# Kernel tuning notes

Measured on AMD Instinct MI355X. Metric: run time of the kernel, lower is better.

The kernel has to match this reference:

```python
import jax, jax.numpy as jnp
import numpy as np

N_HOST, N_FLOW, E = 20000, 200000, 600000
D_IN, D_H, D_OUT = 64, 128, 32
NEG_SLOPE = 0.01  # F.leaky_relu default


def setup_inputs() -> dict:
    key = jax.random.key(0)
    ks = jax.random.split(key, 20)

    def w(k, shape):
        # kaiming-uniform-ish init scale (matches Linear fan-in scaling)
        lim = 1.0 / np.sqrt(shape[0])
        return jax.random.uniform(k, shape, jnp.float32, -lim, lim)

    return {
        "x_host": jax.random.normal(ks[0], (N_HOST, D_IN), jnp.float32),
        "x_flow": jax.random.normal(ks[1], (N_FLOW, D_IN), jnp.float32),
        "src_hf": jax.random.randint(ks[2], (E,), 0, N_HOST, dtype=jnp.int32),
        "dst_hf": jax.random.randint(ks[3], (E,), 0, N_FLOW, dtype=jnp.int32),
        "src_fh": jax.random.randint(ks[4], (E,), 0, N_FLOW, dtype=jnp.int32),
        "dst_fh": jax.random.randint(ks[5], (E,), 0, N_HOST, dtype=jnp.int32),
        "W0_hf_l": w(ks[6], (D_IN, D_H)), "W0_hf_r": w(ks[7], (D_IN, D_H)),
        "b0_hf": jnp.zeros((D_H,), jnp.float32),
        "W0_fh_l": w(ks[8], (D_IN, D_H)), "W0_fh_r": w(ks[9], (D_IN, D_H)),
        "b0_fh": jnp.zeros((D_H,), jnp.float32),
        "W1_hf_l": w(ks[10], (D_H, D_H)), "W1_hf_r": w(ks[11], (D_H, D_H)),
        "b1_hf": jnp.zeros((D_H,), jnp.float32),
        "W1_fh_l": w(ks[12], (D_H, D_H)), "W1_fh_r": w(ks[13], (D_H, D_H)),
        "b1_fh": jnp.zeros((D_H,), jnp.float32),
        "W_out": w(ks[14], (D_H, D_OUT)),
        "b_out": jnp.zeros((D_OUT,), jnp.float32),
    }


def _seg_mean(x, src, dst, n_dst):
    """Mean-aggregate src-node features over edges into n_dst segments."""
    s = jax.ops.segment_sum(x[src], dst, num_segments=n_dst)      # [n_dst, d]
    cnt = jax.ops.segment_sum(jnp.ones(src.shape, x.dtype), dst, num_segments=n_dst)
    return s / jnp.clip(cnt, 1.0)[:, None]


def _sage(x_src, x_dst, src, dst, Wl, Wr, b, n_dst):
    # SAGEConv: lin_l(mean_agg) + bias + lin_r(x_dst)
    agg = _seg_mean(x_src, src, dst, n_dst)
    return agg @ Wl + b + x_dst @ Wr


def reference(x_host, x_flow, src_hf, dst_hf, src_fh, dst_fh,
              W0_hf_l, W0_hf_r, b0_hf, W0_fh_l, W0_fh_r, b0_fh,
              W1_hf_l, W1_hf_r, b1_hf, W1_fh_l, W1_fh_r, b1_fh,
              W_out, b_out):
    lrelu = lambda v: jnp.where(v > 0, v, NEG_SLOPE * v)

    # layer 0
    h_flow = lrelu(_sage(x_host, x_flow, src_hf, dst_hf, W0_hf_l, W0_hf_r, b0_hf, N_FLOW))
    h_host = lrelu(_sage(x_flow, x_host, src_fh, dst_fh, W0_fh_l, W0_fh_r, b0_fh, N_HOST))

    # layer 1
    g_flow = lrelu(_sage(h_host, h_flow, src_hf, dst_hf, W1_hf_l, W1_hf_r, b1_hf, N_FLOW))
    g_host = lrelu(_sage(h_flow, h_host, src_fh, dst_fh, W1_fh_l, W1_fh_r, b1_fh, N_HOST))
    del g_host  # computed (matches module) but only 'flow' feeds the head

    return g_flow @ W_out + b_out  # [N_FLOW, D_OUT]
```

## Files before the change

### kernel.cpp

```cpp
#include <hip/hip_runtime.h>


#define N_HOST 20000
#define N_FLOW 200000
#define NEDGE  600000
#define D_IN   64
#define D_H    128
#define D_OUT  32
#define NSEG   (N_FLOW + N_HOST)
#define NBKT_F 196
#define NBKT_H 79
#define NBKT   (NBKT_F + NBKT_H)
#define NEB    586

typedef unsigned short u16;
typedef unsigned int   u32;
typedef short bf16x8 __attribute__((ext_vector_type(8)));
typedef float f32x4  __attribute__((ext_vector_type(4)));

__device__ __forceinline__ float bfh(u16 h) { return __uint_as_float(((u32)h) << 16); }
__device__ __forceinline__ u16 fbh(float f) {
    u32 u = __float_as_uint(f);
    return (u16)((u + 0x7fffu + ((u >> 16) & 1u)) >> 16);
}
__device__ __forceinline__ u32 packbf(float x, float y) {
    return (u32)fbh(x) | ((u32)fbh(y) << 16);
}
__device__ __forceinline__ void acc8(float* a, uint4 u) {
    a[0] += __uint_as_float(u.x << 16);
    a[1] += __uint_as_float(u.x & 0xffff0000u);
    a[2] += __uint_as_float(u.y << 16);
    a[3] += __uint_as_float(u.y & 0xffff0000u);
    a[4] += __uint_as_float(u.z << 16);
    a[5] += __uint_as_float(u.z & 0xffff0000u);
    a[6] += __uint_as_float(u.w << 16);
    a[7] += __uint_as_float(u.w & 0xffff0000u);
}

__device__ __forceinline__ uint4 gmean(const u16* __restrict__ pool, int rs, int coff,
                                       const int* __restrict__ gcsr,
                                       const int* __restrict__ lcsr, int st0, bool fit,
                                       int st, int en) {
    float a[8] = {0.f, 0.f, 0.f, 0.f, 0.f, 0.f, 0.f, 0.f};
    for (int e = st; e < en; e += 4) {
        int n[4];
#pragma unroll
        for (int j = 0; j < 4; j++)
            n[j] = (e + j < en) ? (fit ? lcsr[e + j - st0] : gcsr[e + j]) : -1;
        uint4 u[4];
#pragma unroll
        for (int j = 0; j < 4; j++)
            u[j] = (n[j] >= 0) ? *(const uint4*)(pool + n[j] * rs + coff)
                               : make_uint4(0u, 0u, 0u, 0u);
#pragma unroll
        for (int j = 0; j < 4; j++) acc8(a, u[j]);
    }
    float inv = (en > st) ? 1.f / (float)(en - st) : 0.f;
    uint4 o;
    o.x = packbf(a[0] * inv, a[1] * inv);
    o.y = packbf(a[2] * inv, a[3] * inv);
    o.z = packbf(a[4] * inv, a[5] * inv);
    o.w = packbf(a[6] * inv, a[7] * inv);
    return o;
}

__global__ void k_pre(const float* __restrict__ W0_hf_l, const float* __restrict__ W0_hf_r,
                      const float* __restrict__ W0_fh_l, const float* __restrict__ W0_fh_r,
                      const float* __restrict__ W1_l, const float* __restrict__ W1_r,
                      const float* __restrict__ Wout,
                      u16* __restrict__ WT0_hf, u16* __restrict__ WT0_fh,
                      u16* __restrict__ WT1_l, u16* __restrict__ WT1_r,
                      u16* __restrict__ WTo,
                      const float* __restrict__ xf, const float* __restrict__ xh,
                      u16* __restrict__ xfb, u16* __restrict__ xhb,
                      const int* __restrict__ dst_hf, const int* __restrict__ dst_fh,
                      int* __restrict__ bcnt) {
    int b = blockIdx.x, t = threadIdx.x;
    if (b < 34) {
        u16 tmp[8];
        if (b < 32) {
            int e = (b & 7) * 2048 + t * 8;
            int n = e >> 7, k0 = e & 127;
            if (b < 8) {
#pragma unroll
                for (int j = 0; j < 8; j++) {
                    int k = k0 + j;
                    tmp[j] = fbh(k < 64 ? W0_hf_l[k * D_H + n] : W0_hf_r[(k - 64) * D_H + n]);
                }
                *(uint4*)(WT0_hf + n * 128 + k0) = *(uint4*)tmp;
            } else if (b < 16) {
#pragma unroll
                for (int j = 0; j < 8; j++) {
                    int k = k0 + j;
                    tmp[j] = fbh(k < 64 ? W0_fh_l[k * D_H + n] : W0_fh_r[(k - 64) * D_H + n]);
                }
                *(uint4*)(WT0_fh + n * 128 + k0) = *(uint4*)tmp;
            } else if (b < 24) {
#pragma unroll
                for (int j = 0; j < 8; j++) tmp[j] = fbh(W1_l[(k0 + j) * D_H + n]);
                *(uint4*)(WT1_l + n * 128 + k0) = *(uint4*)tmp;
            } else {
#pragma unroll
                for (int j = 0; j < 8; j++) tmp[j] = fbh(W1_r[(k0 + j) * D_H + n]);
                *(uint4*)(WT1_r + n * 128 + k0) = *(uint4*)tmp;
            }
        } else {
            int e = (b - 32) * 2048 + t * 8;
            int n = e >> 7, k0 = e & 127;
#pragma unroll
            for (int j = 0; j < 8; j++) tmp[j] = fbh(Wout[(k0 + j) * D_OUT + n]);
            *(uint4*)(WTo + n * 128 + k0) = *(uint4*)tmp;
        }
    } else if (b < 34 + 6875) {
        int q = (b - 34) * 256 + t;
        const int TF = (N_FLOW * D_IN) / 8;
        const int TT = TF + (N_HOST * D_IN) / 8;
        if (q >= TT) return;
        const float* src; u16* dst; int base;
        if (q < TF) { src = xf; dst = xfb; base = q * 8; }
        else        { src = xh; dst = xhb; base = (q - TF) * 8; }
        float4 f0 = *(const float4*)(src + base);
        float4 f1 = *(const float4*)(src + base + 4);
        uint4 o;
        o.x = packbf(f0.x, f0.y); o.y = packbf(f0.z, f0.w);
        o.z = packbf(f1.x, f1.y); o.w = packbf(f1.z, f1.w);
        *(uint4*)(dst + base) = o;
    } else {
        __shared__ int h[NBKT];
        for (int j = t; j < NBKT; j += 256) h[j] = 0;
        __syncthreads();
        int base = (b - 34 - 6875) * 2048;
#pragma unroll
        for (int i = 0; i < 8; i++) {
            int e = base + t + i * 256;
            if (e < 2 * NEDGE) {
                int bkt = (e < NEDGE) ? (dst_hf[e] >> 10)
                                      : (NBKT_F + (dst_fh[e - NEDGE] >> 8));
                atomicAdd(&h[bkt], 1);
            }
        }
        __syncthreads();
        for (int j = t; j < NBKT; j += 256)
            if (h[j]) atomicAdd(&bcnt[j], h[j]);
    }
}

__global__ void kb2(const int* __restrict__ src_hf, const int* __restrict__ dst_hf,
                    const int* __restrict__ src_fh, const int* __restrict__ dst_fh,
                    const int* __restrict__ bcnt, int* __restrict__ bcur,
                    int2* __restrict__ binE) {
    __shared__ int sp[512];
    __shared__ int lh[NBKT];
    __shared__ int lb[NBKT];
    int t = threadIdx.x;
    int o1 = (t < NBKT) ? bcnt[t] : 0;
    int o2 = (t + 256 < NBKT) ? bcnt[t + 256] : 0;
    sp[t] = o1; sp[t + 256] = o2;
    for (int j = t; j < NBKT; j += 256) lh[j] = 0;
    __syncthreads();
    for (int d = 1; d < 512; d <<= 1) {
        int a0 = (t >= d) ? sp[t - d] : 0;
        int a1 = sp[t + 256 - d];
        __syncthreads();
        sp[t] += a0; sp[t + 256] += a1;
        __syncthreads();
    }
    sp[t] -= o1; sp[t + 256] -= o2;
    __syncthreads();
    int base = blockIdx.x * 2048;
    int mybkt[8], myrank[8], mysrc[8], mydst[8];
#pragma unroll
    for (int i = 0; i < 8; i++) {
        int e = base + t + i * 256;
        mybkt[i] = -1;
        if (e < 2 * NEDGE) {
            int s, d;
            if (e < NEDGE) { s = src_hf[e]; d = dst_hf[e]; }
            else           { s = src_fh[e - NEDGE]; d = dst_fh[e - NEDGE] + N_FLOW; }
            int bkt = (d < N_FLOW) ? (d >> 10) : (NBKT_F + ((d - N_FLOW) >> 8));
            mybkt[i] = bkt; mysrc[i] = s; mydst[i] = d;
            myrank[i] = atomicAdd(&lh[bkt], 1);
        }
    }
    __syncthreads();
    for (int j = t; j < NBKT; j += 256)
        lb[j] = lh[j] ? atomicAdd(&bcur[j], lh[j]) : 0;
    __syncthreads();
#pragma unroll
    for (int i = 0; i < 8; i++) {
        if (mybkt[i] >= 0) {
            int pos = sp[mybkt[i]] + lb[mybkt[i]] + myrank[i];
            binE[pos] = make_int2(mysrc[i], mydst[i]);
        }
    }
}

__global__ __launch_bounds__(256) void kb3(const int2* __restrict__ binE,
                                           const int* __restrict__ bcnt,
                                           int* __restrict__ off, int* __restrict__ csr) {
    __shared__ int sp[512];
    __shared__ int deg[1024];
    __shared__ int ts[256];
    int b = blockIdx.x, t = threadIdx.x;
    sp[t] = (t < NBKT) ? bcnt[t] : 0;
    sp[t + 256] = (t + 256 < NBKT) ? bcnt[t + 256] : 0;
    __syncthreads();
    for (int d = 1; d < 512; d <<= 1) {
        int a0 = (t >= d) ? sp[t - d] : 0;
        int a1 = sp[t + 256 - d];
        __syncthreads();
        sp[t] += a0; sp[t + 256] += a1;
        __syncthreads();
    }
    int e0 = (b == 0) ? 0 : sp[b - 1];
    int e1 = sp[b];
    int nbase, ncnt;
    if (b < NBKT_F) { nbase = b << 10; ncnt = min(1024, N_FLOW - nbase); }
    else { nbase = N_FLOW + ((b - NBKT_F) << 8); ncnt = min(256, NSEG - nbase); }
    for (int i = t; i < 1024; i += 256) deg[i] = 0;
    __syncthreads();
    for (int e = e0 + t; e < e1; e += 256) {
        int2 p = binE[e];
        atomicAdd(&deg[p.y - nbase], 1);
    }
    __syncthreads();
    int loc[4]; int s = 0;
#pragma unroll
    for (int j = 0; j < 4; j++) { loc[j] = s; s += deg[t * 4 + j]; }
    ts[t] = s;
    __syncthreads();
    for (int d = 1; d < 256; d <<= 1) {
        int x = (t >= d) ? ts[t - d] : 0;
        __syncthreads();
        ts[t] += x;
        __syncthreads();
    }
    int base2 = e0 + ts[t] - s;
    int dsave[4];
#pragma unroll
    for (int j = 0; j < 4; j++) dsave[j] = deg[t * 4 + j];
    __syncthreads();
#pragma unroll
    for (int j = 0; j < 4; j++) {
        int idx = t * 4 + j;
        int st = base2 + loc[j];
        deg[idx] = st;
        if (idx < ncnt) off[nbase + idx] = st + dsave[j];
    }
    __syncthreads();
    for (int e = e0 + t; e < e1; e += 256) {
        int2 p = binE[e];
        int r = atomicAdd(&deg[p.y - nbase], 1);
        csr[r] = p.x;
    }
}

__global__ __launch_bounds__(256) void k_host(
    const u16* __restrict__ xfb, const u16* __restrict__ xhb,
    const int* __restrict__ off, const int* __restrict__ csr,
    const u16* __restrict__ WT0, const float* __restrict__ b0,
    const u16* __restrict__ WT1l, u16* __restrict__ hT, int M) {
    __shared__ __align__(16) u16 sA[64 * 136];
    __shared__ int sOff[72];
    __shared__ int sCsr[2560];
    const int t = threadIdx.x;
    const int m0 = blockIdx.x * 64;
    if (t < 65) {
        int idx = N_FLOW + m0 - 1 + t;
        sOff[t] = off[min(idx, NSEG - 1)];
    }
#pragma unroll
    for (int i = 0; i < 2; i++) {
        int q = t + i * 256;
        int r = q >> 3, c = q & 7;
        int row = m0 + r;
        uint4 v = make_uint4(0u, 0u, 0u, 0u);
        if (row < M) v = *(const uint4*)(xhb + row * 64 + c * 8);
        *(uint4*)(&sA[r * 136 + 64 + c * 8]) = v;
    }
    __syncthreads();
    int st0 = sOff[0];
    int win = sOff[64] - st0;
    bool fit = (win <= 2560);
    if (fit) for (int e = t; e < win; e += 256) sCsr[e] = csr[st0 + e];
    __syncthreads();
#pragma unroll
    for (int i = 0; i < 2; i++) {
        int q = t + i * 256;
        int r = q >> 3, c = q & 7;
        int row = m0 + r;
        uint4 o = make_uint4(0u, 0u, 0u, 0u);
        if (row < M) o = gmean(xfb, 64, c * 8, csr, sCsr, st0, fit, sOff[r], sOff[r + 1]);
        *(uint4*)(&sA[r * 136 + c * 8]) = o;
    }
    __syncthreads();
    const int w = t >> 6, ln = t & 63, l15 = ln & 15, quad = ln >> 4;
    const u16* pA = sA + (w * 16 + l15) * 136 + quad * 8;
    const u16* pB0 = WT0 + l15 * 128 + quad * 8;
    f32x4 acc[8];
#pragma unroll
    for (int tt = 0; tt < 8; tt++) acc[tt] = (f32x4){0.f, 0.f, 0.f, 0.f};
#pragma unroll
    for (int s = 0; s < 4; s++) {
        bf16x8 a = *(const bf16x8*)(pA + s * 32);
#pragma unroll
        for (int tt = 0; tt < 8; tt++) {
            bf16x8 b = *(const bf16x8*)(pB0 + tt * 2048 + s * 32);
            acc[tt] = __builtin_amdgcn_mfma_f32_16x16x32_bf16(a, b, acc[tt], 0, 0, 0);
        }
    }
#pragma unroll
    for (int tt = 0; tt < 8; tt++) {
        int col = tt * 16 + l15;
        float bv = b0[col];
#pragma unroll
        for (int i = 0; i < 4; i++) {
            int rl = w * 16 + quad * 4 + i;
            float v = acc[tt][i] + bv;
            v = v > 0.f ? v : 0.01f * v;
            sA[rl * 136 + col] = fbh(v);
        }
    }
    const u16* pB1 = WT1l + l15 * 128 + quad * 8;
    f32x4 accB[8];
#pragma unroll
    for (int tt = 0; tt < 8; tt++) accB[tt] = (f32x4){0.f, 0.f, 0.f, 0.f};
#pragma unroll
    for (int s = 0; s < 4; s++) {
        bf16x8 a = *(const bf16x8*)(pA + s * 32);
#pragma unroll
        for (int tt = 0; tt < 8; tt++) {
            bf16x8 b = *(const bf16x8*)(pB1 + tt * 2048 + s * 32);
            accB[tt] = __builtin_amdgcn_mfma_f32_16x16x32_bf16(a, b, accB[tt], 0, 0, 0);
        }
    }
#pragma unroll
    for (int tt = 0; tt < 8; tt++) {
        int col = tt * 16 + l15;
#pragma unroll
        for (int i = 0; i < 4; i++) {
            int row = m0 + w * 16 + quad * 4 + i;
            if (row < M) hT[row * D_H + col] = fbh(accB[tt][i]);
        }
    }
}

__global__ __launch_bounds__(256) void k_mega(
    const u16* __restrict__ xfb, const u16* __restrict__ xhb,
    const int* __restrict__ off, const int* __restrict__ csr,
    const u16* __restrict__ hT,
    const u16* __restrict__ WT0, const float* __restrict__ b0,
    const u16* __restrict__ WT1r, const float* __restrict__ b1,
    const u16* __restrict__ WTo, const float* __restrict__ bout,
    float* __restrict__ OUT) {
    __shared__ __align__(16) u16 sA[64 * 136];
    __shared__ __align__(16) u16 sAg[64 * 136];
    __shared__ int sOff[72];
    __shared__ int sCsr[1024];
    const int t = threadIdx.x;
    const int m0 = blockIdx.x * 64;
    if (t < 65) {
        int idx = m0 - 1 + t;
        sOff[t] = (idx < 0) ? 0 : off[idx];
    }
#pragma unroll
    for (int i = 0; i < 2; i++) {
        int q = t + i * 256;
        int r = q >> 3, c = q & 7;
        int row = m0 + r;
        uint4 v = *(const uint4*)(xfb + row * 64 + c * 8);
        *(uint4*)(&sA[r * 136 + 64 + c * 8]) = v;
    }
    __syncthreads();
    int st0 = sOff[0];
    int win = sOff[64] - st0;
    bool fit = (win <= 1024);
    if (fit) for (int e = t; e < win; e += 256) sCsr[e] = csr[st0 + e];
    __syncthreads();
#pragma unroll
    for (int i = 0; i < 2; i++) {
        int q = t + i * 256;
        int r = q >> 3, c = q & 7;
        uint4 o = gmean(xhb, 64, c * 8, csr, sCsr, st0, fit, sOff[r], sOff[r + 1]);
        *(uint4*)(&sA[r * 136 + c * 8]) = o;
    }
#pragma unroll
    for (int i = 0; i < 4; i++) {
        int q = t + i * 256;
        int r = q >> 4, c = q & 15;
        uint4 o = gmean(hT, 128, c * 8, csr, sCsr, st0, fit, sOff[r], sOff[r + 1]);
        *(uint4*)(&sAg[r * 136 + c * 8]) = o;
    }
    __syncthreads();
    const int w = t >> 6, ln = t & 63, l15 = ln & 15, quad = ln >> 4;
    const u16* pA = sA + (w * 16 + l15) * 136 + quad * 8;
    const u16* pB0 = WT0 + l15 * 128 + quad * 8;
    f32x4 acc[8];
#pragma unroll
    for (int tt = 0; tt < 8; tt++) acc[tt] = (f32x4){0.f, 0.f, 0.f, 0.f};
#pragma unroll
    for (int s = 0; s < 4; s++) {
        bf16x8 a = *(const bf16x8*)(pA + s * 32);
#pragma unroll
        for (int tt = 0; tt < 8; tt++) {
            bf16x8 b = *(const bf16x8*)(pB0 + tt * 2048 + s * 32);
            acc[tt] = __builtin_amdgcn_mfma_f32_16x16x32_bf16(a, b, acc[tt], 0, 0, 0);
        }
    }
#pragma unroll
    for (int tt = 0; tt < 8; tt++) {
        int col = tt * 16 + l15;
        float bv = b0[col];
#pragma unroll
        for (int i = 0; i < 4; i++) {
            int rl = w * 16 + quad * 4 + i;
            float v = acc[tt][i] + bv;
            v = v > 0.f ? v : 0.01f * v;
            sA[rl * 136 + col] = fbh(v);
        }
    }
    const u16* pB1 = WT1r + l15 * 128 + quad * 8;
    f32x4 accB[8];
#pragma unroll
    for (int tt = 0; tt < 8; tt++) accB[tt] = (f32x4){0.f, 0.f, 0.f, 0.f};
#pragma unroll
    for (int s = 0; s < 4; s++) {
        bf16x8 a = *(const bf16x8*)(pA + s * 32);
#pragma unroll
        for (int tt = 0; tt < 8; tt++) {
            bf16x8 b = *(const bf16x8*)(pB1 + tt * 2048 + s * 32);
            accB[tt] = __builtin_amdgcn_mfma_f32_16x16x32_bf16(a, b, accB[tt], 0, 0, 0);
        }
    }
#pragma unroll
    for (int tt = 0; tt < 8; tt++) {
        int col = tt * 16 + l15;
        float bv = b1[col];
#pragma unroll
        for (int i = 0; i < 4; i++) {
            int rl = w * 16 + quad * 4 + i;
            float v = accB[tt][i] + bfh(sAg[rl * 136 + col]) + bv;
            v = v > 0.f ? v : 0.01f * v;
            sA[rl * 136 + col] = fbh(v);
        }
    }
    const u16* pBo = WTo + l15 * 128 + quad * 8;
    f32x4 acc2[2];
    acc2[0] = (f32x4){0.f, 0.f, 0.f, 0.f};
    acc2[1] = (f32x4){0.f, 0.f, 0.f, 0.f};
#pragma unroll
    for (int s = 0; s < 4; s++) {
        bf16x8 g = *(const bf16x8*)(pA + s * 32);
        acc2[0] = __builtin_amdgcn_mfma_f32_16x16x32_bf16(g, *(const bf16x8*)(pBo + s * 32), acc2[0], 0, 0, 0);
        acc2[1] = __builtin_amdgcn_mfma_f32_16x16x32_bf16(g, *(const bf16x8*)(pBo + 2048 + s * 32), acc2[1], 0, 0, 0);
    }
#pragma unroll
    for (int tt = 0; tt < 2; tt++) {
        int col = tt * 16 + l15;
        float bv = bout[col];
#pragma unroll
        for (int i = 0; i < 4; i++) {
            int row = m0 + w * 16 + quad * 4 + i;
            OUT[row * D_OUT + col] = acc2[tt][i] + bv;
        }
    }
}

extern "C" void kernel_launch(void* const* d_in, const int* in_sizes, int n_in,
                              void* d_out, int out_size, void* d_ws, size_t ws_size,
                              hipStream_t stream) {
    const float* x_host  = (const float*)d_in[0];
    const float* x_flow  = (const float*)d_in[1];
    const int* src_hf  = (const int*)d_in[2];
    const int* dst_hf  = (const int*)d_in[3];
    const int* src_fh  = (const int*)d_in[4];
    const int* dst_fh  = (const int*)d_in[5];
    const float* W0_hf_l = (const float*)d_in[6];
    const float* W0_hf_r = (const float*)d_in[7];
    const float* b0_hf   = (const float*)d_in[8];
    const float* W0_fh_l = (const float*)d_in[9];
    const float* W0_fh_r = (const float*)d_in[10];
    const float* b0_fh   = (const float*)d_in[11];
    const float* W1_hf_l = (const float*)d_in[12];
    const float* W1_hf_r = (const float*)d_in[13];
    const float* b1_hf   = (const float*)d_in[14];
    const float* W_out   = (const float*)d_in[18];
    const float* b_out   = (const float*)d_in[19];
    float* out = (float*)d_out;

    char* ws = (char*)d_ws;
    int*  off    = (int*)(ws + 0);
    int*  csr    = (int*)(ws + 880000);
    u16*  hT     = (u16*)(ws + 5680000);
    u16*  xfb    = (u16*)(ws + 10800000);
    u16*  xhb    = (u16*)(ws + 36400000);
    int2* binE   = (int2*)(ws + 38960000);
    int*  bcnt   = (int*)(ws + 48560000);
    int*  bcur   = (int*)(ws + 48561280);
    u16*  WT0_hf = (u16*)(ws + 48562560);
    u16*  WT0_fh = (u16*)(ws + 48595328);
    u16*  WT1_l  = (u16*)(ws + 48628096);
    u16*  WT1_r  = (u16*)(ws + 48660864);
    u16*  WTo    = (u16*)(ws + 48693632);

    hipMemsetAsync(bcnt, 0, 2560, stream);
    k_pre<<<34 + 6875 + NEB, 256, 0, stream>>>(
        W0_hf_l, W0_hf_r, W0_fh_l, W0_fh_r, W1_hf_l, W1_hf_r, W_out,
        WT0_hf, WT0_fh, WT1_l, WT1_r, WTo,
        x_flow, x_host, xfb, xhb, dst_hf, dst_fh, bcnt);
    kb2<<<NEB, 256, 0, stream>>>(src_hf, dst_hf, src_fh, dst_fh, bcnt, bcur, binE);
    kb3<<<NBKT, 256, 0, stream>>>(binE, bcnt, off, csr);
    k_host<<<313, 256, 0, stream>>>(xfb, xhb, off, csr, WT0_fh, b0_fh, WT1_l, hT, N_HOST);
    k_mega<<<3125, 256, 0, stream>>>(xfb, xhb, off, csr, hT, WT0_hf, b0_hf,
                                     WT1_r, b1_hf, WTo, b_out, out);
}
```

Before: 355.7 us.

## Double threads per block in host and flow kernels, split GEMM columns across warps

Both fused kernels move from 256 to 512 threads per 64-row tile. Each thread now gathers one 8-column chunk instead of looping over two, and the 8 waves are laid out as 4 row groups by 2 column halves for the MFMA stages. The goal is more memory-level parallelism in the irregular gather phase and more resident waves to hide latency. The cost is extra __syncthreads between stages, because column-split waves now write shared rows that other waves read. The host kernel's gather unroll is also raised to 8.

```diff
diff --git a/kernel.cpp b/kernel.cpp
--- a/kernel.cpp
+++ b/kernel.cpp
@@ -37,23 +37,24 @@
     a[7] += __uint_as_float(u.w & 0xffff0000u);
 }
 
+template <int U>
 __device__ __forceinline__ uint4 gmean(const u16* __restrict__ pool, int rs, int coff,
                                        const int* __restrict__ gcsr,
                                        const int* __restrict__ lcsr, int st0, bool fit,
                                        int st, int en) {
     float a[8] = {0.f, 0.f, 0.f, 0.f, 0.f, 0.f, 0.f, 0.f};
-    for (int e = st; e < en; e += 4) {
-        int n[4];
-#pragma unroll
-        for (int j = 0; j < 4; j++)
+    for (int e = st; e < en; e += U) {
+        int n[U];
+#pragma unroll
+        for (int j = 0; j < U; j++)
             n[j] = (e + j < en) ? (fit ? lcsr[e + j - st0] : gcsr[e + j]) : -1;
-        uint4 u[4];
-#pragma unroll
-        for (int j = 0; j < 4; j++)
+        uint4 u[U];
+#pragma unroll
+        for (int j = 0; j < U; j++)
             u[j] = (n[j] >= 0) ? *(const uint4*)(pool + n[j] * rs + coff)
                                : make_uint4(0u, 0u, 0u, 0u);
 #pragma unroll
-        for (int j = 0; j < 4; j++) acc8(a, u[j]);
+        for (int j = 0; j < U; j++) acc8(a, u[j]);
     }
     float inv = (en > st) ? 1.f / (float)(en - st) : 0.f;
     uint4 o;
@@ -255,7 +256,7 @@
     }
 }
 
-__global__ __launch_bounds__(256) void k_host(
+__global__ __launch_bounds__(512, 4) void k_host(
     const u16* __restrict__ xfb, const u16* __restrict__ xhb,
     const int* __restrict__ off, const int* __restrict__ csr,
     const u16* __restrict__ WT0, const float* __restrict__ b0,
@@ -269,10 +270,8 @@
         int idx = N_FLOW + m0 - 1 + t;
         sOff[t] = off[min(idx, NSEG - 1)];
     }
-#pragma unroll
-    for (int i = 0; i < 2; i++) {
-        int q = t + i * 256;
-        int r = q >> 3, c = q & 7;
+    {
+        int r = t >> 3, c = t & 7;
         int row = m0 + r;
         uint4 v = make_uint4(0u, 0u, 0u, 0u);
         if (row < M) v = *(const uint4*)(xhb + row * 64 + c * 8);
@@ -282,70 +281,71 @@
     int st0 = sOff[0];
     int win = sOff[64] - st0;
     bool fit = (win <= 2560);
-    if (fit) for (int e = t; e < win; e += 256) sCsr[e] = csr[st0 + e];
-    __syncthreads();
-#pragma unroll
-    for (int i = 0; i < 2; i++) {
-        int q = t + i * 256;
-        int r = q >> 3, c = q & 7;
+    if (fit) for (int e = t; e < win; e += 512) sCsr[e] = csr[st0 + e];
+    __syncthreads();
+    {
+        int r = t >> 3, c = t & 7;
         int row = m0 + r;
         uint4 o = make_uint4(0u, 0u, 0u, 0u);
-        if (row < M) o = gmean(xfb, 64, c * 8, csr, sCsr, st0, fit, sOff[r], sOff[r + 1]);
+        if (row < M) o = gmean<8>(xfb, 64, c * 8, csr, sCsr, st0, fit, sOff[r], sOff[r + 1]);
         *(uint4*)(&sA[r * 136 + c * 8]) = o;
     }
     __syncthreads();
-    const int w = t >> 6, ln = t & 63, l15 = ln & 15, quad = ln >> 4;
-    const u16* pA = sA + (w * 16 + l15) * 136 + quad * 8;
-    const u16* pB0 = WT0 + l15 * 128 + quad * 8;
-    f32x4 acc[8];
-#pragma unroll
-    for (int tt = 0; tt < 8; tt++) acc[tt] = (f32x4){0.f, 0.f, 0.f, 0.f};
+    const int w = t >> 6, wr = w >> 1, wc = w & 1;
+    const int ln = t & 63, l15 = ln & 15, quad = ln >> 4;
+    const u16* pA = sA + (wr * 16 + l15) * 136 + quad * 8;
+    const u16* pB0 = WT0 + wc * 8192 + l15 * 128 + quad * 8;
+    f32x4 acc[4];
+#pragma unroll
+    for (int tt = 0; tt < 4; tt++) acc[tt] = (f32x4){0.f, 0.f, 0.f, 0.f};
 #pragma unroll
     for (int s = 0; s < 4; s++) {
         bf16x8 a = *(const bf16x8*)(pA + s * 32);
 #pragma unroll
-        for (int tt = 0; tt < 8; tt++) {
+        for (int tt = 0; tt < 4; tt++) {
             bf16x8 b = *(const bf16x8*)(pB0 + tt * 2048 + s * 32);
             acc[tt] = __builtin_amdgcn_mfma_f32_16x16x32_bf16(a, b, acc[tt], 0, 0, 0);
         }
     }
-#pragma unroll
-    for (int tt = 0; tt < 8; tt++) {
-        int col = tt * 16 + l15;
+    __syncthreads();
+#pragma unroll
+    for (int tt = 0; tt < 4; tt++) {
+        int col = wc * 64 + tt * 16 + l15;
         float bv = b0[col];
 #pragma unroll
         for (int i = 0; i < 4; i++) {
-            int rl = w * 16 + quad * 4 + i;
+            int rl = wr * 16 + quad * 4 + i;
             float v = acc[tt][i] + bv;
             v = v > 0.f ? v : 0.01f * v;
             sA[rl * 136 + col] = fbh(v);
         }
     }
-    const u16* pB1 = WT1l + l15 * 128 + quad * 8;
-    f32x4 accB[8];
-#pragma unroll
-    for (int tt = 0; tt < 8; tt++) accB[tt] = (f32x4){0.f, 0.f, 0.f, 0.f};
+    __syncthreads();
+    const u16* pB1 = WT1l + wc * 8192 + l15 * 128 + quad * 8;
+    f32x4 accB[4];
+#pragma unroll
+    for (int tt = 0; tt < 4; tt++) accB[tt] = (f32x4){0.f, 0.f, 0.f, 0.f};
 #pragma unroll
     for (int s = 0; s < 4; s++) {
         bf16x8 a = *(const bf16x8*)(pA + s * 32);
 #pragma unroll
-        for (int tt = 0; tt < 8; tt++) {
+        for (int tt = 0; tt < 4; tt++) {
             bf16x8 b = *(const bf16x8*)(pB1 + tt * 2048 + s * 32);
             accB[tt] = __builtin_amdgcn_mfma_f32_16x16x32_bf16(a, b, accB[tt], 0, 0, 0);
         }
     }
 #pragma unroll
-    for (int tt = 0; tt < 8; tt++) {
-        int col = tt * 16 + l15;
+    for (int tt = 0; tt < 4; tt++) {
+        int col = wc * 64 + tt * 16 + l15;
 #pragma unroll
         for (int i = 0; i < 4; i++) {
-            int row = m0 + w * 16 + quad * 4 + i;
+            int row = m0 + wr * 16 + quad * 4 + i;
             if (row < M) hT[row * D_H + col] = fbh(accB[tt][i]);
         }
     }
 }
 
-__global__ __launch_bounds__(256) void k_mega(
+__global__ __launch_bounds__(512, 8) void k_mega(
     const u16* __restrict__ xfb, const u16* __restrict__ xhb,
     const int* __restrict__ off, const int* __restrict__ csr,
     const u16* __restrict__ hT,
@@ -363,105 +363,102 @@
         int idx = m0 - 1 + t;
         sOff[t] = (idx < 0) ? 0 : off[idx];
     }
-#pragma unroll
-    for (int i = 0; i < 2; i++) {
-        int q = t + i * 256;
-        int r = q >> 3, c = q & 7;
-        int row = m0 + r;
-        uint4 v = *(const uint4*)(xfb + row * 64 + c * 8);
+    {
+        int r = t >> 3, c = t & 7;
+        uint4 v = *(const uint4*)(xfb + (m0 + r) * 64 + c * 8);
         *(uint4*)(&sA[r * 136 + 64 + c * 8]) = v;
     }
     __syncthreads();
     int st0 = sOff[0];
     int win = sOff[64] - st0;
     bool fit = (win <= 1024);
-    if (fit) for (int e = t; e < win; e += 256) sCsr[e] = csr[st0 + e];
-    __syncthreads();
+    if (fit) for (int e = t; e < win; e += 512) sCsr[e] = csr[st0 + e];
+    __syncthreads();
+    {
+        int r = t >> 3, c = t & 7;
+        uint4 o = gmean<4>(xhb, 64, c * 8, csr, sCsr, st0, fit, sOff[r], sOff[r + 1]);
+        *(uint4*)(&sA[r * 136 + c * 8]) = o;
+    }
 #pragma unroll
     for (int i = 0; i < 2; i++) {
-        int q = t + i * 256;
-        int r = q >> 3, c = q & 7;
-        uint4 o = gmean(xhb, 64, c * 8, csr, sCsr, st0, fit, sOff[r], sOff[r + 1]);
-        *(uint4*)(&sA[r * 136 + c * 8]) = o;
-    }
-#pragma unroll
-    for (int i = 0; i < 4; i++) {
-        int q = t + i * 256;
+        int q = t + i * 512;
         int r = q >> 4, c = q & 15;
-        uint4 o = gmean(hT, 128, c * 8, csr, sCsr, st0, fit, sOff[r], sOff[r + 1]);
+        uint4 o = gmean<4>(hT, 128, c * 8, csr, sCsr, st0, fit, sOff[r], sOff[r + 1]);
         *(uint4*)(&sAg[r * 136 + c * 8]) = o;
     }
     __syncthreads();
-    const int w = t >> 6, ln = t & 63, l15 = ln & 15, quad = ln >> 4;
-    const u16* pA = sA + (w * 16 + l15) * 136 + quad * 8;
-    const u16* pB0 = WT0 + l15 * 128 + quad * 8;
-    f32x4 acc[8];
-#pragma unroll
-    for (int tt = 0; tt < 8; tt++) acc[tt] = (f32x4){0.f, 0.f, 0.f, 0.f};
+    const int w = t >> 6, wr = w >> 1, wc = w & 1;
+    const int ln = t & 63, l15 = ln & 15, quad = ln >> 4;
+    const u16* pA = sA + (wr * 16 + l15) * 136 + quad * 8;
+    const u16* pB0 = WT0 + wc * 8192 + l15 * 128 + quad * 8;
+    f32x4 acc[4];
+#pragma unroll
+    for (int tt = 0; tt < 4; tt++) acc[tt] = (f32x4){0.f, 0.f, 0.f, 0.f};
 #pragma unroll
     for (int s = 0; s < 4; s++) {
         bf16x8 a = *(const bf16x8*)(pA + s * 32);
 #pragma unroll
-        for (int tt = 0; tt < 8; tt++) {
+        for (int tt = 0; tt < 4; tt++) {
             bf16x8 b = *(const bf16x8*)(pB0 + tt * 2048 + s * 32);
             acc[tt] = __builtin_amdgcn_mfma_f32_16x16x32_bf16(a, b, acc[tt], 0, 0, 0);
         }
     }
-#pragma unroll
-    for (int tt = 0; tt < 8; tt++) {
-        int col = tt * 16 + l15;
+    __syncthreads();
+#pragma unroll
+    for (int tt = 0; tt < 4; tt++) {
+        int col = wc * 64 + tt * 16 + l15;
         float bv = b0[col];
 #pragma unroll
         for (int i = 0; i < 4; i++) {
-            int rl = w * 16 + quad * 4 + i;
+            int rl = wr * 16 + quad * 4 + i;
             float v = acc[tt][i] + bv;
             v = v > 0.f ? v : 0.01f * v;
             sA[rl * 136 + col] = fbh(v);
         }
     }
-    const u16* pB1 = WT1r + l15 * 128 + quad * 8;
-    f32x4 accB[8];
-#pragma unroll
-    for (int tt = 0; tt < 8; tt++) accB[tt] = (f32x4){0.f, 0.f, 0.f, 0.f};
+    __syncthreads();
+    const u16* pB1 = WT1r + wc * 8192 + l15 * 128 + quad * 8;
+    f32x4 accB[4];
+#pragma unroll
+    for (int tt = 0; tt < 4; tt++) accB[tt] = (f32x4){0.f, 0.f, 0.f, 0.f};
 #pragma unroll
     for (int s = 0; s < 4; s++) {
         bf16x8 a = *(const bf16x8*)(pA + s * 32);
 #pragma unroll
-        for (int tt = 0; tt < 8; tt++) {
+        for (int tt = 0; tt < 4; tt++) {
             bf16x8 b = *(const bf16x8*)(pB1 + tt * 2048 + s * 32);
             accB[tt] = __builtin_amdgcn_mfma_f32_16x16x32_bf16(a, b, accB[tt], 0, 0, 0);
         }
     }
 #pragma unroll
-    for (int tt = 0; tt < 8; tt++) {
-        int col = tt * 16 + l15;
+    for (int tt = 0; tt < 4; tt++) {
+        int col = wc * 64 + tt * 16 + l15;
         float bv = b1[col];
 #pragma unroll
         for (int i = 0; i < 4; i++) {
-            int rl = w * 16 + quad * 4 + i;
+            int rl = wr * 16 + quad * 4 + i;
             float v = accB[tt][i] + bfh(sAg[rl * 136 + col]) + bv;
             v = v > 0.f ? v : 0.01f * v;
-            sA[rl * 136 + col] = fbh(v);
-        }
-    }
-    const u16* pBo = WTo + l15 * 128 + quad * 8;
-    f32x4 acc2[2];
-    acc2[0] = (f32x4){0.f, 0.f, 0.f, 0.f};
-    acc2[1] = (f32x4){0.f, 0.f, 0.f, 0.f};
+            sAg[rl * 136 + col] = fbh(v);
+        }
+    }
+    __syncthreads();
+    const u16* pG = sAg + (wr * 16 + l15) * 136 + quad * 8;
+    const u16* pBo = WTo + wc * 2048 + l15 * 128 + quad * 8;
+    f32x4 acc2 = (f32x4){0.f, 0.f, 0.f, 0.f};
 #pragma unroll
     for (int s = 0; s < 4; s++) {
-        bf16x8 g = *(const bf16x8*)(pA + s * 32);
-        acc2[0] = __builtin_amdgcn_mfma_f32_16x16x32_bf16(g, *(const bf16x8*)(pBo + s * 32), acc2[0], 0, 0, 0);
-        acc2[1] = __builtin_amdgcn_mfma_f32_16x16x32_bf16(g, *(const bf16x8*)(pBo + 2048 + s * 32), acc2[1], 0, 0, 0);
-    }
-#pragma unroll
-    for (int tt = 0; tt < 2; tt++) {
-        int col = tt * 16 + l15;
+        bf16x8 g = *(const bf16x8*)(pG + s * 32);
+        bf16x8 b = *(const bf16x8*)(pBo + s * 32);
+        acc2 = __builtin_amdgcn_mfma_f32_16x16x32_bf16(g, b, acc2, 0, 0, 0);
+    }
+    {
+        int col = wc * 16 + l15;
         float bv = bout[col];
 #pragma unroll
         for (int i = 0; i < 4; i++) {
-            int row = m0 + w * 16 + quad * 4 + i;
-            OUT[row * D_OUT + col] = acc2[tt][i] + bv;
+            int row = m0 + wr * 16 + quad * 4 + i;
+            OUT[row * D_OUT + col] = acc2[i] + bv;
         }
     }
 }
@@ -510,7 +507,7 @@
         x_flow, x_host, xfb, xhb, dst_hf, dst_fh, bcnt);
     kb2<<<NEB, 256, 0, stream>>>(src_hf, dst_hf, src_fh, dst_fh, bcnt, bcur, binE);
     kb3<<<NBKT, 256, 0, stream>>>(binE, bcnt, off, csr);
-    k_host<<<313, 256, 0, stream>>>(xfb, xhb, off, csr, WT0_fh, b0_fh, WT1_l, hT, N_HOST);
-    k_mega<<<3125, 256, 0, stream>>>(xfb, xhb, off, csr, hT, WT0_hf, b0_hf,
+    k_host<<<313, 512, 0, stream>>>(xfb, xhb, off, csr, WT0_fh, b0_fh, WT1_l, hT, N_HOST);
+    k_mega<<<3125, 512, 0, stream>>>(xfb, xhb, off, csr, hT, WT0_hf, b0_hf,
                                      WT1_r, b1_hf, WTo, b_out, out);
 }
```

After: 344.2 us. 1.03x faster.
